# Kernel tuning notes

Measured on AMD Instinct MI355X. Metric: run time of the kernel, lower is better.

Reference implementation:

```python
import jax, jax.numpy as jnp
import numpy as np

N = 50000      # nodes
E = 800000     # edges (avg degree 16)
F_IN = 128
HID = 128
C = 40
EPS = 1e-5     # BatchNorm1d eps


def setup_inputs() -> dict:
    key = jax.random.key(0)
    ks = jax.random.split(key, 8)

    def glorot(k, shape):
        lim = np.sqrt(6.0 / (shape[0] + shape[1])).astype(np.float32)
        return jax.random.uniform(k, shape, jnp.float32, -lim, lim)

    inp = {
        "features": jax.random.normal(ks[0], (N, F_IN), jnp.float32),
        "edge_index": jax.random.randint(ks[1], (2, E), 0, N, jnp.int32),
        "W1": glorot(ks[2], (F_IN, HID)), "b1": jnp.zeros((HID,), jnp.float32),
        "gamma1": jnp.ones((HID,), jnp.float32), "beta1": jnp.zeros((HID,), jnp.float32),
        "W2": glorot(ks[3], (HID, HID)), "b2": jnp.zeros((HID,), jnp.float32),
        "gamma2": jnp.ones((HID,), jnp.float32), "beta2": jnp.zeros((HID,), jnp.float32),
        "W3": glorot(ks[4], (HID, C)), "b3": jnp.zeros((C,), jnp.float32),
    }
    return inp


def _gcn_norm(edge_index):
    # Add self-loops and compute symmetric normalization D^-1/2 (A+I) D^-1/2
    loops = jnp.arange(N, dtype=edge_index.dtype)
    src = jnp.concatenate([edge_index[0], loops])
    dst = jnp.concatenate([edge_index[1], loops])
    deg = jax.ops.segment_sum(jnp.ones((E + N,), jnp.float32), dst, num_segments=N)
    dinv = jax.lax.rsqrt(jnp.maximum(deg, 1.0))
    return src, dst, dinv[src] * dinv[dst]  # per-edge norm coefficient


def _gcn_conv(x, W, b, src, dst, norm):
    h = x @ W                                   # [N, out]
    msg = h[src] * norm[:, None]                # gather + scale, [E+N, out]
    return jax.ops.segment_sum(msg, dst, num_segments=N) + b


def _bn(x, gamma, beta):
    # training-mode BatchNorm1d over the node axis (biased variance)
    mu = jnp.mean(x, axis=0)
    var = jnp.mean(jnp.square(x - mu), axis=0)
    return (x - mu) * jax.lax.rsqrt(var + EPS) * gamma + beta


def reference(features, edge_index, W1, b1, gamma1, beta1, W2, b2, gamma2, beta2, W3, b3):
    src, dst, norm = _gcn_norm(edge_index)
    h = jax.nn.relu(_bn(_gcn_conv(features, W1, b1, src, dst, norm), gamma1, beta1))
    h = jax.nn.relu(_bn(_gcn_conv(h, W2, b2, src, dst, norm), gamma2, beta2))
    h = _gcn_conv(h, W3, b3, src, dst, norm)
    return jax.nn.log_softmax(h, axis=-1)
```

## Files before the change

kernel.cpp:

```cpp
#include <hip/hip_runtime.h>
#include <math.h>

#define FEAT 128
#define NCLS 40
#define BN_EPS 1e-5f
#define CAP 64

typedef unsigned short u16;
typedef unsigned int u32;
typedef __attribute__((ext_vector_type(8))) short bf16x8;
typedef __attribute__((ext_vector_type(4))) float f32x4;

__device__ inline u32 f2b2(float a, float b) {
    u32 ua = __float_as_uint(a), ub = __float_as_uint(b);
    ua = (ua + 0x7fffu + ((ua >> 16) & 1u)) >> 16;
    ub = (ub + 0x7fffu + ((ub >> 16) & 1u)) >> 16;
    return ua | (ub << 16);
}
__device__ inline u16 f2b1(float a) {
    u32 ua = __float_as_uint(a);
    return (u16)((ua + 0x7fffu + ((ua >> 16) & 1u)) >> 16);
}
__device__ inline float b2f(u16 u) { return __uint_as_float((u32)u << 16); }
__device__ inline float blo(u32 u) { return __uint_as_float(u << 16); }
__device__ inline float bhi(u32 u) { return __uint_as_float(u & 0xffff0000u); }

__device__ inline void b8acc(uint4 u, float w, float* a) {
    a[0] = fmaf(w, blo(u.x), a[0]); a[1] = fmaf(w, bhi(u.x), a[1]);
    a[2] = fmaf(w, blo(u.y), a[2]); a[3] = fmaf(w, bhi(u.y), a[3]);
    a[4] = fmaf(w, blo(u.z), a[4]); a[5] = fmaf(w, bhi(u.z), a[5]);
    a[6] = fmaf(w, blo(u.w), a[6]); a[7] = fmaf(w, bhi(u.w), a[7]);
}


__device__ inline void stage_wt(const float* __restrict__ W, u16* Wt) {
    const float4* W4 = (const float4*)W;
#pragma unroll
    for (int i = 0; i < 16; ++i) {
        int li = threadIdx.x + i * 256;
        int k = li >> 5;
        int n0 = (li & 31) * 4;
        int s = k >> 5, quad = (k >> 3) & 3, koff = k & 7;
        int nt = n0 >> 4, nl0 = n0 & 15;
        int base = ((s * 8 + nt) * 64 + quad * 16) * 8 + koff;
        float4 w = W4[li];
        Wt[base + (nl0 + 0) * 8] = f2b1(w.x);
        Wt[base + (nl0 + 1) * 8] = f2b1(w.y);
        Wt[base + (nl0 + 2) * 8] = f2b1(w.z);
        Wt[base + (nl0 + 3) * 8] = f2b1(w.w);
    }
}

__device__ inline void stage_wt40(const float* __restrict__ W, u16* Wt) {
    for (int e = threadIdx.x; e < 12 * 64 * 8; e += 256) {
        int j = e & 7;
        int lane = (e >> 3) & 63;
        int tile = e >> 9;
        int s = tile / 3, nt = tile % 3;
        int n = nt * 16 + (lane & 15);
        int k = s * 32 + (lane >> 4) * 8 + j;
        float v = (n < NCLS) ? W[k * NCLS + n] : 0.f;
        Wt[e] = f2b1(v);
    }
}

__global__ __launch_bounds__(256) void k_init(
    const float* __restrict__ W1, const float* __restrict__ W2,
    const float* __restrict__ W3, u16* __restrict__ Wg,
    const int* __restrict__ edges, u32* __restrict__ ebuf,
    int* __restrict__ bucketCnt, int E, int bcap, float inv8n)
{
    int b = blockIdx.x;
    if (b == 0) stage_wt(W1, Wg);
    else if (b == 1) stage_wt(W2, Wg + 128 * 128);
    else if (b == 2) stage_wt40(W3, Wg + 2 * 128 * 128);
    else {
        __shared__ int hcnt[8];
        __shared__ int hbase[8];
        int t = threadIdx.x;
        if (t < 8) hcnt[t] = 0;
        __syncthreads();

        int e0 = (b - 3) * 2048 + t * 8;
        u32 pk[8]; int bk[8];
        int nval = 0;
        if (e0 + 8 <= E) {
            int4 s0 = *(const int4*)(edges + e0);
            int4 s1 = *(const int4*)(edges + e0 + 4);
            int4 d0 = *(const int4*)(edges + E + e0);
            int4 d1 = *(const int4*)(edges + E + e0 + 4);
            int ss[8] = {s0.x, s0.y, s0.z, s0.w, s1.x, s1.y, s1.z, s1.w};
            int dd[8] = {d0.x, d0.y, d0.z, d0.w, d1.x, d1.y, d1.z, d1.w};
#pragma unroll
            for (int k = 0; k < 8; ++k) {
                pk[k] = (u32)ss[k] | ((u32)dd[k] << 16);
                int bx = (int)((float)dd[k] * inv8n);
                bk[k] = bx > 7 ? 7 : bx;
            }
            nval = 8;
        } else {
#pragma unroll
            for (int k = 0; k < 8; ++k) {
                int e = e0 + k;
                if (e < E) {
                    int s = edges[e], d = edges[E + e];
                    pk[k] = (u32)s | ((u32)d << 16);
                    int bx = (int)((float)d * inv8n);
                    bk[k] = bx > 7 ? 7 : bx;
                    nval = k + 1;
                }
            }
        }
#pragma unroll
        for (int k = 0; k < 8; ++k)
            if (k < nval) atomicAdd(&hcnt[bk[k]], 1);
        __syncthreads();
        if (t < 8) hbase[t] = hcnt[t] ? atomicAdd(&bucketCnt[t], hcnt[t]) : 0;
        __syncthreads();
        if (t < 8) hcnt[t] = 0;
        __syncthreads();
#pragma unroll
        for (int k = 0; k < 8; ++k)
            if (k < nval) {
                int off = atomicAdd(&hcnt[bk[k]], 1);
                ebuf[(size_t)bk[k] * bcap + hbase[bk[k]] + off] = pk[k];
            }
    }
}

__device__ inline void mfma_core(const uint4* __restrict__ wt4, const bf16x8* bfrag,
                                 u16* __restrict__ Y, int node, int M, int nl, int quad) {
    int lane = quad * 16 + nl;
    f32x4 acc[8];
#pragma unroll
    for (int nt = 0; nt < 8; ++nt) acc[nt] = (f32x4){0.f, 0.f, 0.f, 0.f};
#pragma unroll
    for (int s = 0; s < 4; ++s) {
#pragma unroll
        for (int nt = 0; nt < 8; ++nt) {
            uint4 aw = wt4[(s * 8 + nt) * 64 + lane];
            bf16x8 af = *(bf16x8*)&aw;
            acc[nt] = __builtin_amdgcn_mfma_f32_16x16x32_bf16(af, bfrag[s], acc[nt], 0, 0, 0);
        }
    }
    if (node < M) {
#pragma unroll
        for (int nt = 0; nt < 8; ++nt) {
            uint2 o;
            o.x = f2b2(acc[nt][0], acc[nt][1]);
            o.y = f2b2(acc[nt][2], acc[nt][3]);
            *(uint2*)&Y[(size_t)node * 128 + nt * 16 + quad * 4] = o;
        }
    }
}


__global__ __launch_bounds__(256, 8) void k_l1_fill(
    const float* __restrict__ X, const u16* __restrict__ Wg, u16* __restrict__ Y, int M,
    const u32* __restrict__ ebuf, const int* __restrict__ bucketCnt, int bcap,
    int* __restrict__ cnt, u16* __restrict__ col,
    int gemmBlocks, int C)
{
    if ((int)blockIdx.x < gemmBlocks) {
        int wv = threadIdx.x >> 6;
        int lane = threadIdx.x & 63;
        int nl = lane & 15, quad = lane >> 4;
        int node = blockIdx.x * 64 + wv * 16 + nl;

        bf16x8 bfrag[4];
        if (node < M) {
            const float4* xr = (const float4*)(X + (size_t)node * 128);
#pragma unroll
            for (int s = 0; s < 4; ++s) {
                float4 xa = xr[s * 8 + quad * 2];
                float4 xb = xr[s * 8 + quad * 2 + 1];
                uint4 bu;
                bu.x = f2b2(xa.x, xa.y); bu.y = f2b2(xa.z, xa.w);
                bu.z = f2b2(xb.x, xb.y); bu.w = f2b2(xb.z, xb.w);
                bfrag[s] = *(bf16x8*)&bu;
            }
        } else {
            uint4 z = make_uint4(0, 0, 0, 0);
#pragma unroll
            for (int s = 0; s < 4; ++s) bfrag[s] = *(bf16x8*)&z;
        }
        mfma_core((const uint4*)Wg, bfrag, Y, node, M, nl, quad);
    } else {
        int fb = blockIdx.x - gemmBlocks;
        int part = fb & 7;
        int chunk = fb >> 3;
        int bcnt = bucketCnt[part];
        const u32* be = ebuf + (size_t)part * bcap;
        int step = C << 11;

        for (int e = (chunk << 11) + (int)threadIdx.x * 8; e < bcnt; e += step) {
            if (e + 8 <= bcnt) {
                uint4 p0 = *(const uint4*)(be + e);
                uint4 p1 = *(const uint4*)(be + e + 4);
                u32 pk[8] = {p0.x, p0.y, p0.z, p0.w, p1.x, p1.y, p1.z, p1.w};
#pragma unroll
                for (int k = 0; k < 8; ++k) {
                    int d = (int)(pk[k] >> 16);
                    int c = atomicAdd(&cnt[d], 1);
                    if (c < CAP) col[(size_t)d * CAP + c] = (u16)(pk[k] & 0xffffu);
                }
            } else {
                for (int q = e; q < bcnt; ++q) {
                    u32 p = be[q];
                    int d = (int)(p >> 16);
                    int c = atomicAdd(&cnt[d], 1);
                    if (c < CAP) col[(size_t)d * CAP + c] = (u16)(p & 0xffffu);
                }
            }
        }
    }
}


__device__ inline void build_bfrag_bn(const u16* __restrict__ X, int node, int M,
                                      int quad, const float* scs, const float* shs,
                                      bf16x8* bfrag) {
    if (node < M) {
        const uint4* xr = (const uint4*)(X + (size_t)node * 128);
#pragma unroll
        for (int s = 0; s < 4; ++s) {
            int k0 = s * 32 + quad * 8;
            uint4 xu = xr[s * 4 + quad];
            float4 sc0 = *(const float4*)&scs[k0];
            float4 sc1 = *(const float4*)&scs[k0 + 4];
            float4 sh0 = *(const float4*)&shs[k0];
            float4 sh1 = *(const float4*)&shs[k0 + 4];
            float v0 = fmaxf(fmaf(blo(xu.x), sc0.x, sh0.x), 0.f);
            float v1 = fmaxf(fmaf(bhi(xu.x), sc0.y, sh0.y), 0.f);
            float v2 = fmaxf(fmaf(blo(xu.y), sc0.z, sh0.z), 0.f);
            float v3 = fmaxf(fmaf(bhi(xu.y), sc0.w, sh0.w), 0.f);
            float v4 = fmaxf(fmaf(blo(xu.z), sc1.x, sh1.x), 0.f);
            float v5 = fmaxf(fmaf(bhi(xu.z), sc1.y, sh1.y), 0.f);
            float v6 = fmaxf(fmaf(blo(xu.w), sc1.z, sh1.z), 0.f);
            float v7 = fmaxf(fmaf(bhi(xu.w), sc1.w, sh1.w), 0.f);
            uint4 bu;
            bu.x = f2b2(v0, v1); bu.y = f2b2(v2, v3);
            bu.z = f2b2(v4, v5); bu.w = f2b2(v6, v7);
            bfrag[s] = *(bf16x8*)&bu;
        }
    } else {
        uint4 z = make_uint4(0, 0, 0, 0);
#pragma unroll
        for (int s = 0; s < 4; ++s) bfrag[s] = *(bf16x8*)&z;
    }
}

__global__ __launch_bounds__(256, 2) void k_mfma_l2(
    const u16* __restrict__ X, const u16* __restrict__ Wg,
    const float* __restrict__ sums, const float* __restrict__ gamma,
    const float* __restrict__ beta, u16* __restrict__ Y, int M)
{
    __shared__ __align__(16) u16 Wt[128 * 128];
    __shared__ __align__(16) float scs[128], shs[128];

    if (threadIdx.x < 128) {
        int f = threadIdx.x;
        float inv_n = 1.f / (float)M;
        float mu = sums[f] * inv_n;
        float var = sums[128 + f] * inv_n - mu * mu;
        float rs = rsqrtf(var + BN_EPS);
        float sc = gamma[f] * rs;
        scs[f] = sc;
        shs[f] = beta[f] - mu * sc;
    }
    {
        uint4* d4 = (uint4*)Wt;
        const uint4* s4 = (const uint4*)Wg;
#pragma unroll
        for (int i = 0; i < 8; ++i) d4[threadIdx.x + i * 256] = s4[threadIdx.x + i * 256];
    }
    __syncthreads();

    int wv = threadIdx.x >> 6;
    int lane = threadIdx.x & 63;
    int nl = lane & 15, quad = lane >> 4;
    int nodeA = blockIdx.x * 128 + wv * 16 + nl;
    int nodeB = nodeA + 64;

    bf16x8 bfragA[4], bfragB[4];
    build_bfrag_bn(X, nodeA, M, quad, scs, shs, bfragA);
    build_bfrag_bn(X, nodeB, M, quad, scs, shs, bfragB);

    const uint4* wt4 = (const uint4*)Wt;
    f32x4 accA[8], accB[8];
#pragma unroll
    for (int nt = 0; nt < 8; ++nt) {
        accA[nt] = (f32x4){0.f, 0.f, 0.f, 0.f};
        accB[nt] = (f32x4){0.f, 0.f, 0.f, 0.f};
    }
#pragma unroll
    for (int s = 0; s < 4; ++s) {
#pragma unroll
        for (int nt = 0; nt < 8; ++nt) {
            uint4 aw = wt4[(s * 8 + nt) * 64 + lane];
            bf16x8 af = *(bf16x8*)&aw;
            accA[nt] = __builtin_amdgcn_mfma_f32_16x16x32_bf16(af, bfragA[s], accA[nt], 0, 0, 0);
            accB[nt] = __builtin_amdgcn_mfma_f32_16x16x32_bf16(af, bfragB[s], accB[nt], 0, 0, 0);
        }
    }
    if (nodeA < M) {
#pragma unroll
        for (int nt = 0; nt < 8; ++nt) {
            uint2 o;
            o.x = f2b2(accA[nt][0], accA[nt][1]);
            o.y = f2b2(accA[nt][2], accA[nt][3]);
            *(uint2*)&Y[(size_t)nodeA * 128 + nt * 16 + quad * 4] = o;
        }
    }
    if (nodeB < M) {
#pragma unroll
        for (int nt = 0; nt < 8; ++nt) {
            uint2 o;
            o.x = f2b2(accB[nt][0], accB[nt][1]);
            o.y = f2b2(accB[nt][2], accB[nt][3]);
            *(uint2*)&Y[(size_t)nodeB * 128 + nt * 16 + quad * 4] = o;
        }
    }
}


__global__ __launch_bounds__(256) void k_mfma_l3(
    const u16* __restrict__ X, const u16* __restrict__ Wg,
    const float* __restrict__ sums, const float* __restrict__ gamma,
    const float* __restrict__ beta, u16* __restrict__ Y, int M)
{
    __shared__ __align__(16) u16 Wt[12 * 64 * 8];
    __shared__ __align__(16) float scs[128], shs[128];

    if (threadIdx.x < 128) {
        int f = threadIdx.x;
        float inv_n = 1.f / (float)M;
        float mu = sums[f] * inv_n;
        float var = sums[128 + f] * inv_n - mu * mu;
        float rs = rsqrtf(var + BN_EPS);
        float sc = gamma[f] * rs;
        scs[f] = sc;
        shs[f] = beta[f] - mu * sc;
    }
    {
        uint4* d4 = (uint4*)Wt;
        const uint4* s4 = (const uint4*)Wg;
#pragma unroll
        for (int i = 0; i < 3; ++i) d4[threadIdx.x + i * 256] = s4[threadIdx.x + i * 256];
    }
    __syncthreads();

    int wv = threadIdx.x >> 6;
    int lane = threadIdx.x & 63;
    int nl = lane & 15, quad = lane >> 4;
    int node = blockIdx.x * 64 + wv * 16 + nl;

    bf16x8 bfrag[4];
    build_bfrag_bn(X, node, M, quad, scs, shs, bfrag);

    const uint4* wt4 = (const uint4*)Wt;
    f32x4 acc[3];
#pragma unroll
    for (int nt = 0; nt < 3; ++nt) acc[nt] = (f32x4){0.f, 0.f, 0.f, 0.f};
#pragma unroll
    for (int s = 0; s < 4; ++s) {
#pragma unroll
        for (int nt = 0; nt < 3; ++nt) {
            uint4 aw = wt4[(s * 3 + nt) * 64 + lane];
            bf16x8 af = *(bf16x8*)&aw;
            acc[nt] = __builtin_amdgcn_mfma_f32_16x16x32_bf16(af, bfrag[s], acc[nt], 0, 0, 0);
        }
    }
    if (node < M) {
#pragma unroll
        for (int nt = 0; nt < 3; ++nt) {
            int c0 = nt * 16 + quad * 4;
            if (c0 < NCLS) {
                uint2 o;
                o.x = f2b2(acc[nt][0], acc[nt][1]);
                o.y = f2b2(acc[nt][2], acc[nt][3]);
                *(uint2*)&Y[(size_t)node * NCLS + c0] = o;
            }
        }
    }
}


__global__ __launch_bounds__(256) void k_agg128_bn(
    const u16* __restrict__ t, const int* __restrict__ cnt,
    const u16* __restrict__ col, const float* __restrict__ bias,
    u16* __restrict__ out, float* __restrict__ sums, int n)
{
    int wid = threadIdx.x >> 4;
    int lane = threadIdx.x & 15;
    float4 bA = ((const float4*)bias)[lane * 2];
    float4 bB = ((const float4*)bias)[lane * 2 + 1];

    float bs[8], bq[8];
#pragma unroll
    for (int k = 0; k < 8; ++k) { bs[k] = 0.f; bq[k] = 0.f; }

    for (int i0 = blockIdx.x * 16; i0 < n; i0 += gridDim.x * 16) {
        int i = i0 + wid;
        if (i < n) {
            int c = cnt[i];
            int deg = c < CAP ? c : CAP;
            int beg = i * CAP, end = beg + deg;
            float di = rsqrtf((float)(c + 1));

            float a[8];
            {
                uint4 su = ((const uint4*)(t + (size_t)i * 128))[lane];
                a[0] = di * blo(su.x); a[1] = di * bhi(su.x);
                a[2] = di * blo(su.y); a[3] = di * bhi(su.y);
                a[4] = di * blo(su.z); a[5] = di * bhi(su.z);
                a[6] = di * blo(su.w); a[7] = di * bhi(su.w);
            }

            for (int j = beg; j < end; j += 8) {
                uint4 c0 = *(const uint4*)(col + j);
                int sr[8] = {
                    (int)(c0.x & 0xffffu), (int)(c0.x >> 16),
                    (int)(c0.y & 0xffffu), (int)(c0.y >> 16),
                    (int)(c0.z & 0xffffu), (int)(c0.z >> 16),
                    (int)(c0.w & 0xffffu), (int)(c0.w >> 16)};
                float w[8]; uint4 v[8];
                if (j + 8 <= end) {
#pragma unroll
                    for (int k = 0; k < 8; ++k) {
                        int sck = cnt[sr[k]];
                        v[k] = ((const uint4*)(t + (size_t)sr[k] * 128))[lane];
                        w[k] = rsqrtf((float)(sck + 1));
                    }
                } else {
#pragma unroll
                    for (int k = 0; k < 8; ++k) {
                        bool valid = (j + k) < end;
                        int s = valid ? sr[k] : 0;
                        int sck = cnt[s];
                        v[k] = ((const uint4*)(t + (size_t)s * 128))[lane];
                        w[k] = valid ? rsqrtf((float)(sck + 1)) : 0.f;
                    }
                }
#pragma unroll
                for (int k = 0; k < 8; ++k) b8acc(v[k], w[k], a);
            }

            float vv[8];
            vv[0] = fmaf(di, a[0], bA.x); vv[1] = fmaf(di, a[1], bA.y);
            vv[2] = fmaf(di, a[2], bA.z); vv[3] = fmaf(di, a[3], bA.w);
            vv[4] = fmaf(di, a[4], bB.x); vv[5] = fmaf(di, a[5], bB.y);
            vv[6] = fmaf(di, a[6], bB.z); vv[7] = fmaf(di, a[7], bB.w);
            uint4 o;
            o.x = f2b2(vv[0], vv[1]); o.y = f2b2(vv[2], vv[3]);
            o.z = f2b2(vv[4], vv[5]); o.w = f2b2(vv[6], vv[7]);
            ((uint4*)(out + (size_t)i * 128))[lane] = o;
#pragma unroll
            for (int k = 0; k < 8; ++k) {
                bs[k] += vv[k];
                bq[k] = fmaf(vv[k], vv[k], bq[k]);
            }
        }
    }

    __shared__ float red[16][128];
#pragma unroll
    for (int k = 0; k < 8; ++k) red[wid][lane * 8 + k] = bs[k];
    __syncthreads();
    if (threadIdx.x < 128) {
        float v = 0.f;
#pragma unroll
        for (int w = 0; w < 16; ++w) v += red[w][threadIdx.x];
        atomicAdd(&sums[threadIdx.x], v);
    }
    __syncthreads();
#pragma unroll
    for (int k = 0; k < 8; ++k) red[wid][lane * 8 + k] = bq[k];
    __syncthreads();
    if (threadIdx.x < 128) {
        float v = 0.f;
#pragma unroll
        for (int w = 0; w < 16; ++w) v += red[w][threadIdx.x];
        atomicAdd(&sums[128 + threadIdx.x], v);
    }
}


__global__ __launch_bounds__(256) void k_agg40(
    const u16* __restrict__ t, const int* __restrict__ cnt,
    const u16* __restrict__ col, const float* __restrict__ bias,
    float* __restrict__ out, int n)
{
    int i = blockIdx.x * 32 + (threadIdx.x >> 3);
    if (i >= n) return;
    int l = threadIdx.x & 7;
    bool act = l < 5;
    int c = cnt[i];
    int deg = c < CAP ? c : CAP;
    int beg = i * CAP, end = beg + deg;
    float di = rsqrtf((float)(c + 1));

    float a[8] = {0.f, 0.f, 0.f, 0.f, 0.f, 0.f, 0.f, 0.f};
    if (act) {
        uint4 su = ((const uint4*)(t + (size_t)i * NCLS))[l];
        a[0] = di * blo(su.x); a[1] = di * bhi(su.x);
        a[2] = di * blo(su.y); a[3] = di * bhi(su.y);
        a[4] = di * blo(su.z); a[5] = di * bhi(su.z);
        a[6] = di * blo(su.w); a[7] = di * bhi(su.w);
    }
    for (int j = beg; j < end; j += 8) {
        uint4 c0 = *(const uint4*)(col + j);
        int sr[8] = {
            (int)(c0.x & 0xffffu), (int)(c0.x >> 16),
            (int)(c0.y & 0xffffu), (int)(c0.y >> 16),
            (int)(c0.z & 0xffffu), (int)(c0.z >> 16),
            (int)(c0.w & 0xffffu), (int)(c0.w >> 16)};
        float w[8]; uint4 v[8];
        if (j + 8 <= end) {
#pragma unroll
            for (int k = 0; k < 8; ++k) {
                int sck = cnt[sr[k]];
                v[k] = act ? ((const uint4*)(t + (size_t)sr[k] * NCLS))[l]
                           : make_uint4(0, 0, 0, 0);
                w[k] = rsqrtf((float)(sck + 1));
            }
        } else {
#pragma unroll
            for (int k = 0; k < 8; ++k) {
                bool valid = (j + k) < end;
                int s = valid ? sr[k] : 0;
                int sck = cnt[s];
                v[k] = act ? ((const uint4*)(t + (size_t)s * NCLS))[l]
                           : make_uint4(0, 0, 0, 0);
                w[k] = valid ? rsqrtf((float)(sck + 1)) : 0.f;
            }
        }
#pragma unroll
        for (int k = 0; k < 8; ++k) b8acc(v[k], w[k], a);
    }

    float v[8];
    float m = -INFINITY;
    if (act) {
        float4 b0 = *(const float4*)(bias + l * 8);
        float4 b1 = *(const float4*)(bias + l * 8 + 4);
        v[0] = fmaf(di, a[0], b0.x); v[1] = fmaf(di, a[1], b0.y);
        v[2] = fmaf(di, a[2], b0.z); v[3] = fmaf(di, a[3], b0.w);
        v[4] = fmaf(di, a[4], b1.x); v[5] = fmaf(di, a[5], b1.y);
        v[6] = fmaf(di, a[6], b1.z); v[7] = fmaf(di, a[7], b1.w);
#pragma unroll
        for (int k = 0; k < 8; ++k) m = fmaxf(m, v[k]);
    }
#pragma unroll
    for (int d = 1; d < 8; d <<= 1) m = fmaxf(m, __shfl_xor(m, d, 8));
    float es = 0.f;
    if (act) {
#pragma unroll
        for (int k = 0; k < 8; ++k) es += expf(v[k] - m);
    }
#pragma unroll
    for (int d = 1; d < 8; d <<= 1) es += __shfl_xor(es, d, 8);
    float ls = logf(es);
    if (act) {
        float4 o0, o1;
        o0.x = v[0] - m - ls; o0.y = v[1] - m - ls;
        o0.z = v[2] - m - ls; o0.w = v[3] - m - ls;
        o1.x = v[4] - m - ls; o1.y = v[5] - m - ls;
        o1.z = v[6] - m - ls; o1.w = v[7] - m - ls;
        *(float4*)(out + (size_t)i * NCLS + l * 8) = o0;
        *(float4*)(out + (size_t)i * NCLS + l * 8 + 4) = o1;
    }
}


extern "C" void kernel_launch(void* const* d_in, const int* in_sizes, int n_in,
                              void* d_out, int out_size, void* d_ws, size_t ws_size,
                              hipStream_t stream) {
    const float* features = (const float*)d_in[0];
    const int* edge_index = (const int*)d_in[1];
    const float* W1 = (const float*)d_in[2];
    const float* b1 = (const float*)d_in[3];
    const float* gamma1 = (const float*)d_in[4];
    const float* beta1 = (const float*)d_in[5];
    const float* W2 = (const float*)d_in[6];
    const float* b2 = (const float*)d_in[7];
    const float* gamma2 = (const float*)d_in[8];
    const float* beta2 = (const float*)d_in[9];
    const float* W3 = (const float*)d_in[10];
    const float* b3 = (const float*)d_in[11];
    float* out = (float*)d_out;

    int n = in_sizes[0] / FEAT;
    int E = in_sizes[1] / 2;

    char* p = (char*)d_ws;
    auto alloc = [&](size_t bytes) -> void* {
        void* r = (void*)p;
        p += (bytes + 255) & ~(size_t)255;
        return r;
    };
    int* cnt       = (int*)alloc((size_t)n * 4);
    float* sums    = (float*)alloc(512 * 4);
    int* bucketCnt = (int*)alloc(8 * 4);
    size_t zspan   = (size_t)((char*)(bucketCnt + 8) - (char*)cnt);
    u16* colb      = (u16*)alloc((size_t)n * CAP * 2 + 64);
    u16* hb        = (u16*)alloc((size_t)n * 128 * 2);
    u16* ab        = (u16*)alloc((size_t)n * 128 * 2);
    u16* wgb       = (u16*)alloc((size_t)(2 * 128 * 128 + 12 * 64 * 8) * 2);
    int bcap       = E / 8 + 16384;
    u32* ebuf      = (u32*)alloc((size_t)8 * bcap * 4);

    float* sums1 = sums;
    float* sums2 = sums + 256;
    u16* Wg1 = wgb;
    u16* Wg2 = wgb + 128 * 128;
    u16* Wg3 = wgb + 2 * 128 * 128;

    int gb64 = (n + 63) / 64;
    int gb128 = (n + 127) / 128;
    int gb16 = (n + 15) / 16;
    int gb32 = (n + 31) / 32;
    int aggGrid = gb16 < 1024 ? gb16 : 1024;
    float inv8n = 8.0f / (float)n;

    hipMemsetAsync(cnt, 0, zspan, stream);

    int nbb = (E + 2047) / 2048;
    k_init<<<3 + nbb, 256, 0, stream>>>(W1, W2, W3, wgb,
                                        edge_index, ebuf, bucketCnt, E, bcap, inv8n);

    int C = 64;
    k_l1_fill<<<gb64 + C * 8, 256, 0, stream>>>(features, Wg1, hb, n,
                                                ebuf, bucketCnt, bcap,
                                                cnt, colb, gb64, C);

    k_agg128_bn<<<aggGrid, 256, 0, stream>>>(hb, cnt, colb, b1, ab, sums1, n);

    k_mfma_l2<<<gb128, 256, 0, stream>>>(ab, Wg2, sums1, gamma1, beta1, hb, n);
    k_agg128_bn<<<aggGrid, 256, 0, stream>>>(hb, cnt, colb, b2, ab, sums2, n);

    k_mfma_l3<<<gb64, 256, 0, stream>>>(ab, Wg3, sums2, gamma2, beta2, hb, n);
    k_agg40<<<gb32, 256, 0, stream>>>(hb, cnt, colb, b3, out, n);
}
```

Before: 299.9 us.

## Process one node per wavefront in 128-wide aggregation with 4-way edge split

Reassigns the 128-feature aggregation kernel so that each 64-lane wavefront handles one node instead of each 16-lane group. The four 16-lane subgroups each gather a different 8-edge chunk, and the partial sums are combined with cross-lane shuffles. The self-loop term is now added after the reduction. This is meant to give more memory-level parallelism per node and fewer serial iterations on high-degree nodes. In exchange, there are a quarter as many nodes in flight per block, lanes sit idle on low-degree nodes (average degree is about 16), and there is extra shuffle work.

```diff
diff --git a/kernel.cpp b/kernel.cpp
--- a/kernel.cpp
+++ b/kernel.cpp
@@ -391,70 +391,73 @@
     const u16* __restrict__ col, const float* __restrict__ bias,
     u16* __restrict__ out, float* __restrict__ sums, int n)
 {
-    int wid = threadIdx.x >> 4;
-    int lane = threadIdx.x & 15;
-    float4 bA = ((const float4*)bias)[lane * 2];
-    float4 bB = ((const float4*)bias)[lane * 2 + 1];
+    int wv = threadIdx.x >> 6;
+    int lane = threadIdx.x & 63;
+    int grp = lane >> 4;
+    int gl = lane & 15;
+    float4 bA = ((const float4*)bias)[gl * 2];
+    float4 bB = ((const float4*)bias)[gl * 2 + 1];
 
     float bs[8], bq[8];
 #pragma unroll
     for (int k = 0; k < 8; ++k) { bs[k] = 0.f; bq[k] = 0.f; }
 
-    for (int i0 = blockIdx.x * 16; i0 < n; i0 += gridDim.x * 16) {
-        int i = i0 + wid;
-        if (i < n) {
-            int c = cnt[i];
-            int deg = c < CAP ? c : CAP;
-            int beg = i * CAP, end = beg + deg;
-            float di = rsqrtf((float)(c + 1));
-
-            float a[8];
-            {
-                uint4 su = ((const uint4*)(t + (size_t)i * 128))[lane];
-                a[0] = di * blo(su.x); a[1] = di * bhi(su.x);
-                a[2] = di * blo(su.y); a[3] = di * bhi(su.y);
-                a[4] = di * blo(su.z); a[5] = di * bhi(su.z);
-                a[6] = di * blo(su.w); a[7] = di * bhi(su.w);
-            }
-
-            for (int j = beg; j < end; j += 8) {
-                uint4 c0 = *(const uint4*)(col + j);
-                int sr[8] = {
-                    (int)(c0.x & 0xffffu), (int)(c0.x >> 16),
-                    (int)(c0.y & 0xffffu), (int)(c0.y >> 16),
-                    (int)(c0.z & 0xffffu), (int)(c0.z >> 16),
-                    (int)(c0.w & 0xffffu), (int)(c0.w >> 16)};
-                float w[8]; uint4 v[8];
-                if (j + 8 <= end) {
-#pragma unroll
-                    for (int k = 0; k < 8; ++k) {
-                        int sck = cnt[sr[k]];
-                        v[k] = ((const uint4*)(t + (size_t)sr[k] * 128))[lane];
-                        w[k] = rsqrtf((float)(sck + 1));
-                    }
-                } else {
-#pragma unroll
-                    for (int k = 0; k < 8; ++k) {
-                        bool valid = (j + k) < end;
-                        int s = valid ? sr[k] : 0;
-                        int sck = cnt[s];
-                        v[k] = ((const uint4*)(t + (size_t)s * 128))[lane];
-                        w[k] = valid ? rsqrtf((float)(sck + 1)) : 0.f;
-                    }
-                }
-#pragma unroll
-                for (int k = 0; k < 8; ++k) b8acc(v[k], w[k], a);
-            }
-
-            float vv[8];
-            vv[0] = fmaf(di, a[0], bA.x); vv[1] = fmaf(di, a[1], bA.y);
-            vv[2] = fmaf(di, a[2], bA.z); vv[3] = fmaf(di, a[3], bA.w);
-            vv[4] = fmaf(di, a[4], bB.x); vv[5] = fmaf(di, a[5], bB.y);
-            vv[6] = fmaf(di, a[6], bB.z); vv[7] = fmaf(di, a[7], bB.w);
+    int widx = blockIdx.x * 4 + wv;
+    int wtotal = gridDim.x * 4;
+
+    for (int i = widx; i < n; i += wtotal) {
+        int c = cnt[i];
+        int deg = c < CAP ? c : CAP;
+        int beg = i * CAP, end = beg + deg;
+        float di = rsqrtf((float)(c + 1));
+
+        float a[8];
+#pragma unroll
+        for (int k = 0; k < 8; ++k) a[k] = 0.f;
+
+        for (int j0 = beg; j0 < end; j0 += 32) {
+            int jg = j0 + grp * 8;
+            uint4 c0 = *(const uint4*)(col + jg);
+            int sr[8] = {
+                (int)(c0.x & 0xffffu), (int)(c0.x >> 16),
+                (int)(c0.y & 0xffffu), (int)(c0.y >> 16),
+                (int)(c0.z & 0xffffu), (int)(c0.z >> 16),
+                (int)(c0.w & 0xffffu), (int)(c0.w >> 16)};
+            float w[8]; uint4 v[8];
+#pragma unroll
+            for (int k = 0; k < 8; ++k) {
+                bool valid = (jg + k) < end;
+                int s = valid ? sr[k] : 0;
+                int sck = cnt[s];
+                v[k] = ((const uint4*)(t + (size_t)s * 128))[gl];
+                w[k] = valid ? rsqrtf((float)(sck + 1)) : 0.f;
+            }
+#pragma unroll
+            for (int k = 0; k < 8; ++k) b8acc(v[k], w[k], a);
+        }
+
+#pragma unroll
+        for (int k = 0; k < 8; ++k) {
+            a[k] += __shfl_xor(a[k], 16, 64);
+            a[k] += __shfl_xor(a[k], 32, 64);
+        }
+
+        uint4 su = ((const uint4*)(t + (size_t)i * 128))[gl];
+        float d2 = di * di;
+        float vv[8];
+        vv[0] = fmaf(di, a[0], fmaf(d2, blo(su.x), bA.x));
+        vv[1] = fmaf(di, a[1], fmaf(d2, bhi(su.x), bA.y));
+        vv[2] = fmaf(di, a[2], fmaf(d2, blo(su.y), bA.z));
+        vv[3] = fmaf(di, a[3], fmaf(d2, bhi(su.y), bA.w));
+        vv[4] = fmaf(di, a[4], fmaf(d2, blo(su.z), bB.x));
+        vv[5] = fmaf(di, a[5], fmaf(d2, bhi(su.z), bB.y));
+        vv[6] = fmaf(di, a[6], fmaf(d2, blo(su.w), bB.z));
+        vv[7] = fmaf(di, a[7], fmaf(d2, bhi(su.w), bB.w));
+        if (grp == 0) {
             uint4 o;
             o.x = f2b2(vv[0], vv[1]); o.y = f2b2(vv[2], vv[3]);
             o.z = f2b2(vv[4], vv[5]); o.w = f2b2(vv[6], vv[7]);
-            ((uint4*)(out + (size_t)i * 128))[lane] = o;
+            ((uint4*)(out + (size_t)i * 128))[gl] = o;
 #pragma unroll
             for (int k = 0; k < 8; ++k) {
                 bs[k] += vv[k];
@@ -463,24 +466,24 @@
         }
     }
 
-    __shared__ float red[16][128];
-#pragma unroll
-    for (int k = 0; k < 8; ++k) red[wid][lane * 8 + k] = bs[k];
+    __shared__ float red[4][128];
+#pragma unroll
+    for (int k = 0; k < 8; ++k)
+        if (grp == 0) red[wv][gl * 8 + k] = bs[k];
     __syncthreads();
     if (threadIdx.x < 128) {
-        float v = 0.f;
-#pragma unroll
-        for (int w = 0; w < 16; ++w) v += red[w][threadIdx.x];
+        float v = red[0][threadIdx.x] + red[1][threadIdx.x]
+                + red[2][threadIdx.x] + red[3][threadIdx.x];
         atomicAdd(&sums[threadIdx.x], v);
     }
     __syncthreads();
 #pragma unroll
-    for (int k = 0; k < 8; ++k) red[wid][lane * 8 + k] = bq[k];
+    for (int k = 0; k < 8; ++k)
+        if (grp == 0) red[wv][gl * 8 + k] = bq[k];
     __syncthreads();
     if (threadIdx.x < 128) {
-        float v = 0.f;
-#pragma unroll
-        for (int w = 0; w < 16; ++w) v += red[w][threadIdx.x];
+        float v = red[0][threadIdx.x] + red[1][threadIdx.x]
+                + red[2][threadIdx.x] + red[3][threadIdx.x];
         atomicAdd(&sums[128 + threadIdx.x], v);
     }
 }
@@ -618,9 +621,10 @@
 
     int gb64 = (n + 63) / 64;
     int gb128 = (n + 127) / 128;
-    int gb16 = (n + 15) / 16;
     int gb32 = (n + 31) / 32;
-    int aggGrid = gb16 < 1024 ? gb16 : 1024;
+    int aggGrid = 1024;
+    int nwaves4 = (n + 3) / 4;
+    if (nwaves4 < aggGrid) aggGrid = nwaves4;
     float inv8n = 8.0f / (float)n;
 
     hipMemsetAsync(cnt, 0, zspan, stream);
```

Result: slower. 347.1 us (+15.7%).

## Sort nodes by degree to balance aggregation warps

Applied to the files above, without the earlier changes.

Adds a counting sort of nodes by in-degree (histogram, serial scan, scatter) that produces a permutation. The three aggregation kernels then process nodes in that order, so the 16-lane groups in a wavefront handle nodes of similar degree and loop divergence is reduced. The cost is three extra small kernel launches plus an indirection per node, and gather locality on the output and self rows is lost because neighbouring groups now touch scattered node rows. The u16 permutation assumes n fits in 16 bits, which the existing u16 column encoding already relies on.

```diff
diff --git a/kernel.cpp b/kernel.cpp
--- a/kernel.cpp
+++ b/kernel.cpp
@@ -213,6 +213,35 @@
                 }
             }
         }
+    }
+}
+
+
+__global__ __launch_bounds__(256) void k_hist(const int* __restrict__ cnt,
+                                              int* __restrict__ dcnt, int n) {
+    int i = blockIdx.x * 256 + threadIdx.x;
+    if (i < n) {
+        int d = cnt[i]; d = d < CAP ? d : CAP;
+        atomicAdd(&dcnt[d], 1);
+    }
+}
+
+__global__ __launch_bounds__(64) void k_scan(const int* __restrict__ dcnt,
+                                             int* __restrict__ dpos) {
+    if (threadIdx.x == 0) {
+        int s = 0;
+        for (int d = 0; d <= CAP; ++d) { dpos[d] = s; s += dcnt[d]; }
+    }
+}
+
+__global__ __launch_bounds__(256) void k_scatter(const int* __restrict__ cnt,
+                                                 int* __restrict__ dpos,
+                                                 u16* __restrict__ perm, int n) {
+    int i = blockIdx.x * 256 + threadIdx.x;
+    if (i < n) {
+        int d = cnt[i]; d = d < CAP ? d : CAP;
+        int pos = atomicAdd(&dpos[d], 1);
+        perm[pos] = (u16)i;
     }
 }
 
@@ -388,7 +417,8 @@
 
 __global__ __launch_bounds__(256) void k_agg128_bn(
     const u16* __restrict__ t, const int* __restrict__ cnt,
-    const u16* __restrict__ col, const float* __restrict__ bias,
+    const u16* __restrict__ col, const u16* __restrict__ perm,
+    const float* __restrict__ bias,
     u16* __restrict__ out, float* __restrict__ sums, int n)
 {
     int wid = threadIdx.x >> 4;
@@ -401,8 +431,9 @@
     for (int k = 0; k < 8; ++k) { bs[k] = 0.f; bq[k] = 0.f; }
 
     for (int i0 = blockIdx.x * 16; i0 < n; i0 += gridDim.x * 16) {
-        int i = i0 + wid;
-        if (i < n) {
+        int idx = i0 + wid;
+        if (idx < n) {
+            int i = (int)perm[idx];
             int c = cnt[i];
             int deg = c < CAP ? c : CAP;
             int beg = i * CAP, end = beg + deg;
@@ -488,11 +519,13 @@
 
 __global__ __launch_bounds__(256) void k_agg40(
     const u16* __restrict__ t, const int* __restrict__ cnt,
-    const u16* __restrict__ col, const float* __restrict__ bias,
+    const u16* __restrict__ col, const u16* __restrict__ perm,
+    const float* __restrict__ bias,
     float* __restrict__ out, int n)
 {
-    int i = blockIdx.x * 32 + (threadIdx.x >> 3);
-    if (i >= n) return;
+    int idx = blockIdx.x * 32 + (threadIdx.x >> 3);
+    if (idx >= n) return;
+    int i = (int)perm[idx];
     int l = threadIdx.x & 7;
     bool act = l < 5;
     int c = cnt[i];
@@ -602,8 +635,11 @@
     int* cnt       = (int*)alloc((size_t)n * 4);
     float* sums    = (float*)alloc(512 * 4);
     int* bucketCnt = (int*)alloc(8 * 4);
-    size_t zspan   = (size_t)((char*)(bucketCnt + 8) - (char*)cnt);
+    int* dcnt      = (int*)alloc(72 * 4);
+    size_t zspan   = (size_t)((char*)(dcnt + 72) - (char*)cnt);
+    int* dpos      = (int*)alloc(72 * 4);
     u16* colb      = (u16*)alloc((size_t)n * CAP * 2 + 64);
+    u16* permb     = (u16*)alloc((size_t)n * 2 + 64);
     u16* hb        = (u16*)alloc((size_t)n * 128 * 2);
     u16* ab        = (u16*)alloc((size_t)n * 128 * 2);
     u16* wgb       = (u16*)alloc((size_t)(2 * 128 * 128 + 12 * 64 * 8) * 2);
@@ -620,6 +656,7 @@
     int gb128 = (n + 127) / 128;
     int gb16 = (n + 15) / 16;
     int gb32 = (n + 31) / 32;
+    int gb256 = (n + 255) / 256;
     int aggGrid = gb16 < 1024 ? gb16 : 1024;
     float inv8n = 8.0f / (float)n;
 
@@ -634,11 +671,15 @@
                                                 ebuf, bucketCnt, bcap,
                                                 cnt, colb, gb64, C);
 
-    k_agg128_bn<<<aggGrid, 256, 0, stream>>>(hb, cnt, colb, b1, ab, sums1, n);
+    k_hist<<<gb256, 256, 0, stream>>>(cnt, dcnt, n);
+    k_scan<<<1, 64, 0, stream>>>(dcnt, dpos);
+    k_scatter<<<gb256, 256, 0, stream>>>(cnt, dpos, permb, n);
+
+    k_agg128_bn<<<aggGrid, 256, 0, stream>>>(hb, cnt, colb, permb, b1, ab, sums1, n);
 
     k_mfma_l2<<<gb128, 256, 0, stream>>>(ab, Wg2, sums1, gamma1, beta1, hb, n);
-    k_agg128_bn<<<aggGrid, 256, 0, stream>>>(hb, cnt, colb, b2, ab, sums2, n);
+    k_agg128_bn<<<aggGrid, 256, 0, stream>>>(hb, cnt, colb, permb, b2, ab, sums2, n);
 
     k_mfma_l3<<<gb64, 256, 0, stream>>>(ab, Wg3, sums2, gamma2, beta2, hb, n);
-    k_agg40<<<gb32, 256, 0, stream>>>(hb, cnt, colb, b3, out, n);
-}
+    k_agg40<<<gb32, 256, 0, stream>>>(hb, cnt, colb, permb, b3, out, n);
+}
```

New measurement: 554.6 us. 1.85x slower.
